# Optimization experiments

Measured on AMD Instinct MI355X. Metric: run time of the kernel, lower is better.

Reference implementation:

```python
import jax, jax.numpy as jnp
import numpy as np

H, W, C = 56, 56, 192
WS, SS = 7, 3          # window_size, shift_size
NH, HD = 6, 32         # num_heads, head_dim
N = WS * WS            # tokens per window = 49
HIDDEN = 4 * C
EPS = 1e-5


def _rel_pos_index():
    coords = np.stack(np.meshgrid(np.arange(WS), np.arange(WS), indexing='ij'))  # (2,ws,ws)
    flat = coords.reshape(2, -1)
    rel = flat[:, :, None] - flat[:, None, :]            # (2,N,N)
    rel = rel.transpose(1, 2, 0)
    rel[:, :, 0] += WS - 1
    rel[:, :, 1] += WS - 1
    rel[:, :, 0] *= 2 * WS - 1
    return rel.sum(-1)                                   # (N,N) int


def _attn_mask():
    img = np.zeros((H, W))
    cnt = 0
    for hs in (slice(0, -WS), slice(-WS, -SS), slice(-SS, None)):
        for ws_ in (slice(0, -WS), slice(-WS, -SS), slice(-SS, None)):
            img[hs, ws_] = cnt
            cnt += 1
    mw = img.reshape(H // WS, WS, W // WS, WS).transpose(0, 2, 1, 3).reshape(-1, N)  # (nW,N)
    diff = mw[:, None, :] - mw[:, :, None]
    return np.where(diff != 0, -100.0, 0.0).astype(np.float32)  # (nW,N,N)


REL_IDX = jnp.asarray(_rel_pos_index())
ATTN_MASK = jnp.asarray(_attn_mask())


def _ln(x, w, b):
    mu = x.mean(-1, keepdims=True)
    var = ((x - mu) ** 2).mean(-1, keepdims=True)
    return (x - mu) * jax.lax.rsqrt(var + EPS) * w + b


def _window_partition(x):
    # (B,H,W,C) -> (B*nW, N, C)
    B = x.shape[0]
    x = x.reshape(B, H // WS, WS, W // WS, WS, C)
    x = x.transpose(0, 1, 3, 2, 4, 5)
    return x.reshape(-1, N, C)


def _window_reverse(win, B):
    # (B*nW, N, C) -> (B,H,W,C)
    x = win.reshape(B, H // WS, W // WS, WS, WS, C)
    x = x.transpose(0, 1, 3, 2, 4, 5)
    return x.reshape(B, H, W, C)


def setup_inputs() -> dict:
    key = jax.random.key(0)
    ks = jax.random.split(key, 16)
    s = 0.02
    return {
        'x': jax.random.normal(ks[0], (64, H * W, C), jnp.float32),
        'norm1_w': jnp.ones((C,), jnp.float32),
        'norm1_b': jnp.zeros((C,), jnp.float32),
        'qkv_w': jax.random.normal(ks[1], (C, 3 * C), jnp.float32) * s,
        'qkv_b': jnp.zeros((3 * C,), jnp.float32),
        'rpb': jax.random.normal(ks[2], ((2 * WS - 1) ** 2, NH), jnp.float32) * s,
        'proj_w': jax.random.normal(ks[3], (C, C), jnp.float32) * s,
        'proj_b': jnp.zeros((C,), jnp.float32),
        'norm2_w': jnp.ones((C,), jnp.float32),
        'norm2_b': jnp.zeros((C,), jnp.float32),
        'fc1_w': jax.random.normal(ks[4], (C, HIDDEN), jnp.float32) * s,
        'fc1_b': jnp.zeros((HIDDEN,), jnp.float32),
        'fc2_w': jax.random.normal(ks[5], (HIDDEN, C), jnp.float32) * s,
        'fc2_b': jnp.zeros((C,), jnp.float32),
    }


def reference(x, norm1_w, norm1_b, qkv_w, qkv_b, rpb, proj_w, proj_b,
              norm2_w, norm2_b, fc1_w, fc1_b, fc2_w, fc2_b):
    B = x.shape[0]
    nW = (H // WS) * (W // WS)
    shortcut = x
    h = _ln(x, norm1_w, norm1_b).reshape(B, H, W, C)
    # cyclic shift
    h = jnp.roll(h, shift=(-SS, -SS), axis=(1, 2))
    xw = _window_partition(h)                                   # (B*nW, N, C)
    # windowed MHA
    qkv = (xw @ qkv_w + qkv_b).reshape(-1, N, 3, NH, HD).transpose(2, 0, 3, 1, 4)
    q, k, v = qkv[0], qkv[1], qkv[2]                            # (Bn, NH, N, HD)
    scale = HD ** -0.5
    attn = jnp.einsum('bhnd,bhmd->bhnm', q * scale, k)          # (Bn, NH, N, N)
    bias = rpb[REL_IDX.reshape(-1)].reshape(N, N, NH).transpose(2, 0, 1)
    attn = attn + bias[None]
    attn = attn.reshape(B, nW, NH, N, N) + ATTN_MASK[None, :, None]
    attn = jax.nn.softmax(attn.reshape(-1, NH, N, N), axis=-1)
    out = jnp.einsum('bhnm,bhmd->bhnd', attn, v)
    out = out.transpose(0, 2, 1, 3).reshape(-1, N, C)
    out = out @ proj_w + proj_b
    # reverse windows + un-shift
    h = _window_reverse(out, B)
    h = jnp.roll(h, shift=(SS, SS), axis=(1, 2)).reshape(B, H * W, C)
    x = shortcut + h
    # MLP (exact GELU, as torch nn.GELU default)
    m = _ln(x, norm2_w, norm2_b)
    m = jax.nn.gelu(m @ fc1_w + fc1_b, approximate=False)
    m = m @ fc2_w + fc2_b
    return x + m
```

## Files before the change

kernel.cpp:

```cpp
#include <hip/hip_runtime.h>
#include <hip/hip_bf16.h>

typedef __hip_bfloat16 bf16;
typedef __attribute__((ext_vector_type(8))) short short8;
typedef __attribute__((ext_vector_type(4))) short short4v;
typedef __attribute__((ext_vector_type(4))) float floatx4;

__device__ __forceinline__ floatx4 mfma16(short8 a, short8 b, floatx4 c) {
  return __builtin_amdgcn_mfma_f32_16x16x32_bf16(a, b, c, 0, 0, 0);
}

__device__ __forceinline__ float wave_sum(float v) {
#pragma unroll
  for (int off = 1; off < 64; off <<= 1) v += __shfl_xor(v, off);
  return v;
}

__device__ __forceinline__ void gload16(const void* g, void* l) {
  __builtin_amdgcn_global_load_lds(
      (const __attribute__((address_space(1))) unsigned int*)g,
      (__attribute__((address_space(3))) unsigned int*)l, 16, 0, 0);
}

__device__ __forceinline__ short8 lds_frag(const char* base, int row, int kb) {
  return *(const short8*)(base + row * 384 + (kb ^ ((row & 7) << 4)));
}
__device__ __forceinline__ short8 lds_frag128(const char* base, int row, int kb) {
  return *(const short8*)(base + row * 128 + (kb ^ ((row & 7) << 4)));
}

__global__ __launch_bounds__(256) void k_wt(const float* __restrict__ w,
                                            bf16* __restrict__ wt, int K, int N) {
  int id = blockIdx.x * 256 + threadIdx.x;
  if (id < K * N) {
    int n = id / K;
    int k = id - n * K;
    wt[id] = __float2bfloat16(w[(long)k * N + n]);
  }
}

template <bool GATHER>
__global__ __launch_bounds__(256) void k_ln(const float* __restrict__ xin,
                                            const float* __restrict__ w,
                                            const float* __restrict__ b,
                                            bf16* __restrict__ out) {
  const int lane = threadIdx.x & 63;
  const long row = (long)blockIdx.x * 4 + (threadIdx.x >> 6);
  long srow;
  if (GATHER) {
    int win = (int)(row / 49);
    int token = (int)(row - (long)win * 49);
    int bimg = win >> 6, wi = (win & 63) >> 3, wj = win & 7;
    int ti = token / 7, tj = token - ti * 7;
    int h = wi * 7 + ti + 3; if (h >= 56) h -= 56;
    int ww = wj * 7 + tj + 3; if (ww >= 56) ww -= 56;
    srow = (long)bimg * 3136 + h * 56 + ww;
  } else {
    srow = row;
  }
  const float* src = xin + srow * 192;
  float v0 = src[lane], v1 = src[lane + 64], v2 = src[lane + 128];
  float mu = wave_sum(v0 + v1 + v2) * (1.f / 192.f);
  float d0 = v0 - mu, d1 = v1 - mu, d2 = v2 - mu;
  float var = wave_sum(d0 * d0 + d1 * d1 + d2 * d2) * (1.f / 192.f);
  float rs = rsqrtf(var + 1e-5f);
  bf16* dst = out + row * 192;
  dst[lane]       = __float2bfloat16(d0 * rs * w[lane] + b[lane]);
  dst[lane + 64]  = __float2bfloat16(d1 * rs * w[lane + 64] + b[lane + 64]);
  dst[lane + 128] = __float2bfloat16(d2 * rs * w[lane + 128] + b[lane + 128]);
}

template <int EPI>
__global__ __launch_bounds__(256, 3) void k_gemm(const bf16* __restrict__ A,
                                                 const bf16* __restrict__ Bt,
                                                 const float* __restrict__ bias,
                                                 bf16* __restrict__ Cbf,
                                                 float* __restrict__ Cfp,
                                                 const float* __restrict__ res,
                                                 int Ncols, int K, long row0) {
  __shared__ __align__(16) char As[64 * 384];
  __shared__ __align__(16) char Bs[64 * 384];
  const int t = threadIdx.x;
  const int lane = t & 63, wid = t >> 6;
  const int lanelo = lane & 15, quad = lane >> 4;
  const long m0 = (long)blockIdx.x * 64;
  const int n0 = blockIdx.y * 64;
  const int wm = (wid >> 1) * 32, wn = (wid & 1) * 32;

  floatx4 acc[2][2];
#pragma unroll
  for (int i = 0; i < 2; i++)
#pragma unroll
    for (int j = 0; j < 2; j++) acc[i][j] = (floatx4){0.f, 0.f, 0.f, 0.f};

  const char* Ab = (const char*)(A + m0 * (long)K);
  const char* Bb = (const char*)(Bt + (long)n0 * K);
  const int ldab = 2 * K;

  for (int k0b = 0; k0b < 2 * K; k0b += 384) {
    __syncthreads();
#pragma unroll
    for (int i = 0; i < 6; i++) {
      int c = i * 256 + t;
      int r = c / 24;
      int j = c - r * 24;
      int be = (j * 16) ^ ((r & 7) << 4);
      gload16(Ab + (long)r * ldab + k0b + be, As + c * 16);
      gload16(Bb + (long)r * ldab + k0b + be, Bs + c * 16);
    }
    __syncthreads();

#pragma unroll
    for (int kk = 0; kk < 6; kk++) {
      const int kb = kk * 64 + quad * 16;
      short8 a0 = lds_frag(As, wm + lanelo, kb);
      short8 a1 = lds_frag(As, wm + 16 + lanelo, kb);
      short8 b0 = lds_frag(Bs, wn + lanelo, kb);
      short8 b1 = lds_frag(Bs, wn + 16 + lanelo, kb);
      acc[0][0] = mfma16(a0, b0, acc[0][0]);
      acc[0][1] = mfma16(a0, b1, acc[0][1]);
      acc[1][0] = mfma16(a1, b0, acc[1][0]);
      acc[1][1] = mfma16(a1, b1, acc[1][1]);
    }
  }

#pragma unroll
  for (int mi = 0; mi < 2; mi++) {
#pragma unroll
    for (int reg = 0; reg < 4; reg++) {
      const long r = m0 + wm + mi * 16 + quad * 4 + reg;
      long orow = r;
      if (EPI == 2) {
        const long rg = row0 + r;
        int win = (int)(rg / 49);
        int token = (int)(rg - (long)win * 49);
        int bimg = win >> 6, wi = (win & 63) >> 3, wj = win & 7;
        int ti = token / 7, tj = token - ti * 7;
        int h = wi * 7 + ti + 3; if (h >= 56) h -= 56;
        int ww = wj * 7 + tj + 3; if (ww >= 56) ww -= 56;
        orow = (long)bimg * 3136 + h * 56 + ww;
      }
#pragma unroll
      for (int ni = 0; ni < 2; ni++) {
        const int c = n0 + wn + ni * 16 + lanelo;
        float v = acc[mi][ni][reg] + bias[c];
        if (EPI == 0) {
          Cbf[r * Ncols + c] = __float2bfloat16(v);
        } else if (EPI == 1) {
          v = 0.5f * v * (1.f + erff(v * 0.70710678118654752f));
          Cbf[r * Ncols + c] = __float2bfloat16(v);
        } else if (EPI == 2) {
          Cfp[orow * 192 + c] = v + res[orow * 192 + c];
        } else {
          Cfp[r * 192 + c] = v + res[r * 192 + c];
        }
      }
    }
  }
}

__global__ __launch_bounds__(256, 2) void k_attn2(const bf16* __restrict__ xw,
                                                  const bf16* __restrict__ wq,
                                                  const float* __restrict__ qkvb,
                                                  const float* __restrict__ rpb,
                                                  bf16* __restrict__ attC) {
  __shared__ __align__(16) bf16 smem[4 * 7424];
  const int t = threadIdx.x, lane = t & 63, wid = t >> 6;
  const int lanelo = lane & 15, quad = lane >> 4;
  const int unit = blockIdx.x * 4 + wid;
  const int win = unit / 6, head = unit - win * 6;
  bf16* Qs = smem + wid * 7424;
  bf16* Ks = Qs + 2560;
  bf16* Vt = Qs + 5120;
  bf16* Ps = Qs;
  const long rowbase = (long)win * 49;

  const int w_in = win & 63, wiw = w_in >> 3, wjw = w_in & 7;
  int cTi[4], cTj[4], cLab[4];
  bool cval[4];
#pragma unroll
  for (int ni = 0; ni < 4; ni++) {
    int j = ni * 16 + lanelo;
    cval[ni] = (j < 49);
    if (j > 48) j = 48;
    int ti = j / 7, tj = j - ti * 7;
    int rr = wiw * 7 + ti, cc = wjw * 7 + tj;
    cTi[ni] = ti; cTj[ni] = tj;
    cLab[ni] = ((rr < 49) ? 0 : (rr < 53 ? 1 : 2)) * 3 +
               ((cc < 49) ? 0 : (cc < 53 ? 1 : 2));
  }

  const float scale = 0.17677669529663687f;

  {
    floatx4 aq[4][6];
#pragma unroll
    for (int mi = 0; mi < 4; mi++)
#pragma unroll
      for (int ni = 0; ni < 6; ni++) aq[mi][ni] = (floatx4){0.f, 0.f, 0.f, 0.f};
#pragma unroll
    for (int kk = 0; kk < 6; kk++) {
      const int kb = kk * 64 + quad * 16;
      short8 af[4];
#pragma unroll
      for (int mi = 0; mi < 4; mi++)
        af[mi] = *(const short8*)((const char*)xw +
                                  (rowbase + mi * 16 + lanelo) * 384 + kb);
#pragma unroll
      for (int ni = 0; ni < 6; ni++) {
        const int wrow = (ni >> 1) * 192 + head * 32 + (ni & 1) * 16 + lanelo;
        short8 bf = *(const short8*)((const char*)wq + (long)wrow * 384 + kb);
#pragma unroll
        for (int mi = 0; mi < 4; mi++) aq[mi][ni] = mfma16(af[mi], bf, aq[mi][ni]);
      }
    }
#pragma unroll
    for (int ni = 0; ni < 6; ni++) {
      const int p = ni >> 1;
      const int d = (ni & 1) * 16 + lanelo;
      const float bb = qkvb[p * 192 + head * 32 + d];
      if (p < 2) {
        bf16* dst = (p == 0) ? Qs : Ks;
#pragma unroll
        for (int mi = 0; mi < 4; mi++)
#pragma unroll
          for (int reg = 0; reg < 4; reg++) {
            int tok = mi * 16 + quad * 4 + reg;
            dst[tok * 40 + d] = __float2bfloat16(aq[mi][ni][reg] + bb);
          }
      } else {
#pragma unroll
        for (int mi = 0; mi < 4; mi++) {
          union { short4v s; bf16 hh[4]; } pv;
#pragma unroll
          for (int reg = 0; reg < 4; reg++)
            pv.hh[reg] = __float2bfloat16(aq[mi][ni][reg] + bb);
          *(short4v*)(&Vt[d * 72 + mi * 16 + quad * 4]) = pv.s;
        }
      }
    }
  }

  float rinv[16];
  {
    floatx4 aS[4][4];
#pragma unroll
    for (int mi = 0; mi < 4; mi++) {
      short8 aqf = *(const short8*)(&Qs[(mi * 16 + lanelo) * 40 + quad * 8]);
#pragma unroll
      for (int ni = 0; ni < 4; ni++) {
        short8 bk = *(const short8*)(&Ks[(ni * 16 + lanelo) * 40 + quad * 8]);
        aS[mi][ni] = mfma16(aqf, bk, (floatx4){0.f, 0.f, 0.f, 0.f});
      }
    }
#pragma unroll
    for (int mi = 0; mi < 4; mi++) {
#pragma unroll
      for (int reg = 0; reg < 4; reg++) {
        int i = mi * 16 + quad * 4 + reg;
        if (i > 48) i = 48;
        int ti = i / 7, tj = i - ti * 7;
        int rr = wiw * 7 + ti, cc = wjw * 7 + tj;
        int rlab = ((rr < 49) ? 0 : (rr < 53 ? 1 : 2)) * 3 +
                   ((cc < 49) ? 0 : (cc < 53 ? 1 : 2));
        float sv[4];
        float mx = -1e30f;
#pragma unroll
        for (int ni = 0; ni < 4; ni++) {
          float s;
          if (cval[ni]) {
            int ridx = (ti - cTi[ni] + 6) * 13 + (tj - cTj[ni] + 6);
            float bb = rpb[ridx * 6 + head];
            if (rlab != cLab[ni]) bb -= 100.f;
            s = aS[mi][ni][reg] * scale + bb;
          } else {
            s = -1e30f;
          }
          sv[ni] = s;
          mx = fmaxf(mx, s);
        }
        mx = fmaxf(mx, __shfl_xor(mx, 1));
        mx = fmaxf(mx, __shfl_xor(mx, 2));
        mx = fmaxf(mx, __shfl_xor(mx, 4));
        mx = fmaxf(mx, __shfl_xor(mx, 8));
        float sum = 0.f;
#pragma unroll
        for (int ni = 0; ni < 4; ni++) {
          float p = __expf(sv[ni] - mx);
          sv[ni] = p;
          sum += p;
        }
        sum += __shfl_xor(sum, 1);
        sum += __shfl_xor(sum, 2);
        sum += __shfl_xor(sum, 4);
        sum += __shfl_xor(sum, 8);
        rinv[mi * 4 + reg] = 1.f / sum;
#pragma unroll
        for (int ni = 0; ni < 4; ni++) aS[mi][ni][reg] = sv[ni];
      }
    }
#pragma unroll
    for (int mi = 0; mi < 4; mi++)
#pragma unroll
      for (int ni = 0; ni < 4; ni++)
#pragma unroll
        for (int reg = 0; reg < 4; reg++)
          Ps[(mi * 16 + quad * 4 + reg) * 72 + ni * 16 + lanelo] =
              __float2bfloat16(aS[mi][ni][reg]);
  }

  floatx4 aO[4][2];
#pragma unroll
  for (int mi = 0; mi < 4; mi++)
#pragma unroll
    for (int ni = 0; ni < 2; ni++) aO[mi][ni] = (floatx4){0.f, 0.f, 0.f, 0.f};
#pragma unroll
  for (int ks = 0; ks < 2; ks++) {
#pragma unroll
    for (int mi = 0; mi < 4; mi++) {
      short8 ap = *(const short8*)(&Ps[(mi * 16 + lanelo) * 72 + ks * 32 + quad * 8]);
#pragma unroll
      for (int ni = 0; ni < 2; ni++) {
        short8 bv = *(const short8*)(&Vt[(ni * 16 + lanelo) * 72 + ks * 32 + quad * 8]);
        aO[mi][ni] = mfma16(ap, bv, aO[mi][ni]);
      }
    }
  }

#pragma unroll
  for (int mi = 0; mi < 4; mi++)
#pragma unroll
    for (int reg = 0; reg < 4; reg++) {
      int i = mi * 16 + quad * 4 + reg;
      if (i < 49) {
        float rv = rinv[mi * 4 + reg];
#pragma unroll
        for (int ni = 0; ni < 2; ni++) {
          int d = ni * 16 + lanelo;
          attC[(rowbase + i) * 192 + head * 32 + d] =
              __float2bfloat16(aO[mi][ni][reg] * rv);
        }
      }
    }
}

__global__ __launch_bounds__(256, 4) void k_mlp(float* xres,
                                                const float* __restrict__ lw,
                                                const float* __restrict__ lb,
                                                const bf16* __restrict__ w1t,
                                                const float* __restrict__ b1,
                                                const bf16* __restrict__ w2t,
                                                const float* __restrict__ b2) {
  __shared__ __align__(16) char As[64 * 384];
  __shared__ __align__(16) char Hs[2][64 * 128];
  const int t = threadIdx.x, lane = t & 63, wid = t >> 6;
  const int lanelo = lane & 15, quad = lane >> 4;
  const long row0 = (long)blockIdx.x * 64;

  for (int i = 0; i < 16; i++) {
    int r = wid * 16 + i;
    const float* src = xres + (row0 + r) * 192;
    float v0 = src[lane], v1 = src[lane + 64], v2 = src[lane + 128];
    float mu = wave_sum(v0 + v1 + v2) * (1.f / 192.f);
    float d0 = v0 - mu, d1 = v1 - mu, d2 = v2 - mu;
    float var = wave_sum(d0 * d0 + d1 * d1 + d2 * d2) * (1.f / 192.f);
    float rs = rsqrtf(var + 1e-5f);
    int sw = (r & 7) << 4;
    *(bf16*)(As + r * 384 + ((2 * lane) ^ sw)) =
        __float2bfloat16(d0 * rs * lw[lane] + lb[lane]);
    *(bf16*)(As + r * 384 + ((128 + 2 * lane) ^ sw)) =
        __float2bfloat16(d1 * rs * lw[lane + 64] + lb[lane + 64]);
    *(bf16*)(As + r * 384 + ((256 + 2 * lane) ^ sw)) =
        __float2bfloat16(d2 * rs * lw[lane + 128] + lb[lane + 128]);
  }

  floatx4 acc2[4][3];
#pragma unroll
  for (int mi = 0; mi < 4; mi++)
#pragma unroll
    for (int ni = 0; ni < 3; ni++) acc2[mi][ni] = (floatx4){0.f, 0.f, 0.f, 0.f};

  __syncthreads();

  const int hcol = wid * 16 + lanelo;
  const int ocol0 = wid * 48;

  for (int nc = 0; nc < 12; nc++) {
    const char* w1p = (const char*)w1t + (long)(nc * 64 + hcol) * 384;
    floatx4 acc1[4];
#pragma unroll
    for (int mi = 0; mi < 4; mi++) acc1[mi] = (floatx4){0.f, 0.f, 0.f, 0.f};
#pragma unroll
    for (int kk = 0; kk < 6; kk++) {
      const int kb = kk * 64 + quad * 16;
      short8 bf = *(const short8*)(w1p + kb);
#pragma unroll
      for (int mi = 0; mi < 4; mi++) {
        short8 af = lds_frag(As, mi * 16 + lanelo, kb);
        acc1[mi] = mfma16(af, bf, acc1[mi]);
      }
    }

    char* H = Hs[nc & 1];
    const float b1v = b1[nc * 64 + hcol];
#pragma unroll
    for (int mi = 0; mi < 4; mi++)
#pragma unroll
      for (int reg = 0; reg < 4; reg++) {
        int r = mi * 16 + quad * 4 + reg;
        float v = acc1[mi][reg] + b1v;
        v = 0.5f * v * (1.f + erff(v * 0.70710678118654752f));
        *(bf16*)(H + r * 128 + ((2 * hcol) ^ ((r & 7) << 4))) =
            __float2bfloat16(v);
      }
    __syncthreads();

#pragma unroll
    for (int ks = 0; ks < 2; ks++) {
      const int kb = ks * 64 + quad * 16;
      short8 ha[4];
#pragma unroll
      for (int mi = 0; mi < 4; mi++)
        ha[mi] = lds_frag128(H, mi * 16 + lanelo, kb);
#pragma unroll
      for (int ni = 0; ni < 3; ni++) {
        short8 bv = *(const short8*)((const char*)w2t +
                                     (long)(ocol0 + ni * 16 + lanelo) * 1536 +
                                     nc * 128 + kb);
#pragma unroll
        for (int mi = 0; mi < 4; mi++)
          acc2[mi][ni] = mfma16(ha[mi], bv, acc2[mi][ni]);
      }
    }
  }

#pragma unroll
  for (int mi = 0; mi < 4; mi++)
#pragma unroll
    for (int ni = 0; ni < 3; ni++) {
      const int c = ocol0 + ni * 16 + lanelo;
      const float b2v = b2[c];
#pragma unroll
      for (int reg = 0; reg < 4; reg++) {
        const long g = (row0 + mi * 16 + quad * 4 + reg) * 192 + c;
        xres[g] = acc2[mi][ni][reg] + b2v + xres[g];
      }
    }
}

extern "C" void kernel_launch(void* const* d_in, const int* in_sizes, int n_in,
                              void* d_out, int out_size, void* d_ws, size_t ws_size,
                              hipStream_t stream) {
  const float* x     = (const float*)d_in[0];
  const float* n1w   = (const float*)d_in[1];
  const float* n1b   = (const float*)d_in[2];
  const float* qkvw  = (const float*)d_in[3];
  const float* qkvb  = (const float*)d_in[4];
  const float* rpb   = (const float*)d_in[5];
  const float* projw = (const float*)d_in[6];
  const float* projb = (const float*)d_in[7];
  const float* n2w   = (const float*)d_in[8];
  const float* n2b   = (const float*)d_in[9];
  const float* fc1w  = (const float*)d_in[10];
  const float* fc1b  = (const float*)d_in[11];
  const float* fc2w  = (const float*)d_in[12];
  const float* fc2b  = (const float*)d_in[13];
  float* outf = (float*)d_out;

  char* ws = (char*)d_ws;
  bf16* xw      = (bf16*)(ws + 0);
  bf16* attC    = (bf16*)(ws + 77070336LL);
  bf16* wt_qkv  = (bf16*)(ws + 154140672LL);
  bf16* wt_proj = (bf16*)(ws + 154140672LL + 221184LL);
  bf16* wt_fc1  = (bf16*)(ws + 154140672LL + 294912LL);
  bf16* wt_fc2  = (bf16*)(ws + 154140672LL + 589824LL);

  k_wt<<<dim3((192 * 576 + 255) / 256), 256, 0, stream>>>(qkvw, wt_qkv, 192, 576);
  k_wt<<<dim3((192 * 192 + 255) / 256), 256, 0, stream>>>(projw, wt_proj, 192, 192);
  k_wt<<<dim3((192 * 768 + 255) / 256), 256, 0, stream>>>(fc1w, wt_fc1, 192, 768);
  k_wt<<<dim3((768 * 192 + 255) / 256), 256, 0, stream>>>(fc2w, wt_fc2, 768, 192);

  k_ln<true><<<dim3(50176), 256, 0, stream>>>(x, n1w, n1b, xw);

  k_attn2<<<dim3(6144), 256, 0, stream>>>(xw, wt_qkv, qkvb, rpb, attC);

  k_gemm<2><<<dim3(3136, 3), 256, 0, stream>>>(attC, wt_proj, projb, nullptr,
                                               outf, x, 192, 192, 0);

  k_mlp<<<dim3(3136), 256, 0, stream>>>(outf, n2w, n2b, wt_fc1, fc1b,
                                        wt_fc2, fc2b);
}
```

Before: 993.1 us.

## Precompute bias+mask tables per window class and split QKV projection into QK and V passes

A new small kernel builds a 64x64 table of relative-position bias plus shift mask (with -inf padding) for each of the 4 window classes and 6 heads. The attention kernel then reads one table entry instead of doing per-element index arithmetic and gathering from rpb. It also splits the fused QKV accumulation into separate QK and V passes, which lowers live accumulator registers but reloads the xw fragments twice. The table is stored in the output buffer as scratch before the output is written.

```diff
diff --git a/kernel.cpp b/kernel.cpp
--- a/kernel.cpp
+++ b/kernel.cpp
@@ -36,6 +36,30 @@
     int n = id / K;
     int k = id - n * K;
     wt[id] = __float2bfloat16(w[(long)k * N + n]);
+  }
+}
+
+__global__ __launch_bounds__(256) void k_bias(const float* __restrict__ rpb,
+                                              float* __restrict__ Btab) {
+  const int bh = blockIdx.x;
+  const int cls = bh / 6, head = bh - cls * 6;
+  const bool rb = (cls & 2) != 0, cb = (cls & 1) != 0;
+  for (int idx = threadIdx.x; idx < 4096; idx += 256) {
+    int i = idx >> 6, j = idx & 63;
+    float v;
+    if (j >= 49) {
+      v = -1e30f;
+    } else {
+      int ie = (i > 48) ? 48 : i;
+      int ti = ie / 7, tj = ie - ti * 7;
+      int cti = j / 7, ctj = j - cti * 7;
+      int ridx = (ti - cti + 6) * 13 + (tj - ctj + 6);
+      v = rpb[ridx * 6 + head];
+      int rlab = (rb ? (ti < 4 ? 1 : 2) : 0) * 3 + (cb ? (tj < 4 ? 1 : 2) : 0);
+      int clab = (rb ? (cti < 4 ? 1 : 2) : 0) * 3 + (cb ? (ctj < 4 ? 1 : 2) : 0);
+      if (rlab != clab) v -= 100.f;
+    }
+    Btab[(long)bh * 4096 + i * 64 + j] = v;
   }
 }
 
@@ -162,7 +186,7 @@
 __global__ __launch_bounds__(256, 2) void k_attn2(const bf16* __restrict__ xw,
                                                   const bf16* __restrict__ wq,
                                                   const float* __restrict__ qkvb,
-                                                  const float* __restrict__ rpb,
+                                                  const float* __restrict__ Btab,
                                                   bf16* __restrict__ attC) {
   __shared__ __align__(16) bf16 smem[4 * 7424];
   const int t = threadIdx.x, lane = t & 63, wid = t >> 6;
@@ -175,29 +199,18 @@
   bf16* Ps = Qs;
   const long rowbase = (long)win * 49;
 
-  const int w_in = win & 63, wiw = w_in >> 3, wjw = w_in & 7;
-  int cTi[4], cTj[4], cLab[4];
-  bool cval[4];
-#pragma unroll
-  for (int ni = 0; ni < 4; ni++) {
-    int j = ni * 16 + lanelo;
-    cval[ni] = (j < 49);
-    if (j > 48) j = 48;
-    int ti = j / 7, tj = j - ti * 7;
-    int rr = wiw * 7 + ti, cc = wjw * 7 + tj;
-    cTi[ni] = ti; cTj[ni] = tj;
-    cLab[ni] = ((rr < 49) ? 0 : (rr < 53 ? 1 : 2)) * 3 +
-               ((cc < 49) ? 0 : (cc < 53 ? 1 : 2));
-  }
+  const int w_in = win & 63;
+  const int cls = (((w_in >> 3) == 7) ? 2 : 0) + (((w_in & 7) == 7) ? 1 : 0);
+  const float* Bt = Btab + (long)(cls * 6 + head) * 4096;
 
   const float scale = 0.17677669529663687f;
 
   {
-    floatx4 aq[4][6];
+    floatx4 aq[4][4];
 #pragma unroll
     for (int mi = 0; mi < 4; mi++)
 #pragma unroll
-      for (int ni = 0; ni < 6; ni++) aq[mi][ni] = (floatx4){0.f, 0.f, 0.f, 0.f};
+      for (int ni = 0; ni < 4; ni++) aq[mi][ni] = (floatx4){0.f, 0.f, 0.f, 0.f};
 #pragma unroll
     for (int kk = 0; kk < 6; kk++) {
       const int kb = kk * 64 + quad * 16;
@@ -207,7 +220,7 @@
         af[mi] = *(const short8*)((const char*)xw +
                                   (rowbase + mi * 16 + lanelo) * 384 + kb);
 #pragma unroll
-      for (int ni = 0; ni < 6; ni++) {
+      for (int ni = 0; ni < 4; ni++) {
         const int wrow = (ni >> 1) * 192 + head * 32 + (ni & 1) * 16 + lanelo;
         short8 bf = *(const short8*)((const char*)wq + (long)wrow * 384 + kb);
 #pragma unroll
@@ -215,28 +228,54 @@
       }
     }
 #pragma unroll
-    for (int ni = 0; ni < 6; ni++) {
+    for (int ni = 0; ni < 4; ni++) {
       const int p = ni >> 1;
       const int d = (ni & 1) * 16 + lanelo;
       const float bb = qkvb[p * 192 + head * 32 + d];
-      if (p < 2) {
-        bf16* dst = (p == 0) ? Qs : Ks;
-#pragma unroll
-        for (int mi = 0; mi < 4; mi++)
-#pragma unroll
-          for (int reg = 0; reg < 4; reg++) {
-            int tok = mi * 16 + quad * 4 + reg;
-            dst[tok * 40 + d] = __float2bfloat16(aq[mi][ni][reg] + bb);
-          }
-      } else {
-#pragma unroll
-        for (int mi = 0; mi < 4; mi++) {
-          union { short4v s; bf16 hh[4]; } pv;
-#pragma unroll
-          for (int reg = 0; reg < 4; reg++)
-            pv.hh[reg] = __float2bfloat16(aq[mi][ni][reg] + bb);
-          *(short4v*)(&Vt[d * 72 + mi * 16 + quad * 4]) = pv.s;
+      bf16* dst = (p == 0) ? Qs : Ks;
+#pragma unroll
+      for (int mi = 0; mi < 4; mi++)
+#pragma unroll
+        for (int reg = 0; reg < 4; reg++) {
+          int tok = mi * 16 + quad * 4 + reg;
+          dst[tok * 40 + d] = __float2bfloat16(aq[mi][ni][reg] + bb);
         }
+    }
+  }
+
+  {
+    floatx4 av[4][2];
+#pragma unroll
+    for (int mi = 0; mi < 4; mi++)
+#pragma unroll
+      for (int ni = 0; ni < 2; ni++) av[mi][ni] = (floatx4){0.f, 0.f, 0.f, 0.f};
+#pragma unroll
+    for (int kk = 0; kk < 6; kk++) {
+      const int kb = kk * 64 + quad * 16;
+      short8 af[4];
+#pragma unroll
+      for (int mi = 0; mi < 4; mi++)
+        af[mi] = *(const short8*)((const char*)xw +
+                                  (rowbase + mi * 16 + lanelo) * 384 + kb);
+#pragma unroll
+      for (int ni = 0; ni < 2; ni++) {
+        const int wrow = 384 + head * 32 + ni * 16 + lanelo;
+        short8 bf = *(const short8*)((const char*)wq + (long)wrow * 384 + kb);
+#pragma unroll
+        for (int mi = 0; mi < 4; mi++) av[mi][ni] = mfma16(af[mi], bf, av[mi][ni]);
+      }
+    }
+#pragma unroll
+    for (int ni = 0; ni < 2; ni++) {
+      const int d = ni * 16 + lanelo;
+      const float bb = qkvb[384 + head * 32 + d];
+#pragma unroll
+      for (int mi = 0; mi < 4; mi++) {
+        union { short4v s; bf16 hh[4]; } pv;
+#pragma unroll
+        for (int reg = 0; reg < 4; reg++)
+          pv.hh[reg] = __float2bfloat16(av[mi][ni][reg] + bb);
+        *(short4v*)(&Vt[d * 72 + mi * 16 + quad * 4]) = pv.s;
       }
     }
   }
@@ -257,25 +296,13 @@
     for (int mi = 0; mi < 4; mi++) {
 #pragma unroll
       for (int reg = 0; reg < 4; reg++) {
-        int i = mi * 16 + quad * 4 + reg;
-        if (i > 48) i = 48;
-        int ti = i / 7, tj = i - ti * 7;
-        int rr = wiw * 7 + ti, cc = wjw * 7 + tj;
-        int rlab = ((rr < 49) ? 0 : (rr < 53 ? 1 : 2)) * 3 +
-                   ((cc < 49) ? 0 : (cc < 53 ? 1 : 2));
+        const int i = mi * 16 + quad * 4 + reg;
+        const float* bp = Bt + i * 64;
         float sv[4];
         float mx = -1e30f;
 #pragma unroll
         for (int ni = 0; ni < 4; ni++) {
-          float s;
-          if (cval[ni]) {
-            int ridx = (ti - cTi[ni] + 6) * 13 + (tj - cTj[ni] + 6);
-            float bb = rpb[ridx * 6 + head];
-            if (rlab != cLab[ni]) bb -= 100.f;
-            s = aS[mi][ni][reg] * scale + bb;
-          } else {
-            s = -1e30f;
-          }
+          float s = aS[mi][ni][reg] * scale + bp[ni * 16 + lanelo];
           sv[ni] = s;
           mx = fmaxf(mx, s);
         }
@@ -474,15 +501,18 @@
   bf16* wt_proj = (bf16*)(ws + 154140672LL + 221184LL);
   bf16* wt_fc1  = (bf16*)(ws + 154140672LL + 294912LL);
   bf16* wt_fc2  = (bf16*)(ws + 154140672LL + 589824LL);
+  float* Btab   = (float*)d_out;
 
   k_wt<<<dim3((192 * 576 + 255) / 256), 256, 0, stream>>>(qkvw, wt_qkv, 192, 576);
   k_wt<<<dim3((192 * 192 + 255) / 256), 256, 0, stream>>>(projw, wt_proj, 192, 192);
   k_wt<<<dim3((192 * 768 + 255) / 256), 256, 0, stream>>>(fc1w, wt_fc1, 192, 768);
   k_wt<<<dim3((768 * 192 + 255) / 256), 256, 0, stream>>>(fc2w, wt_fc2, 768, 192);
 
+  k_bias<<<dim3(24), 256, 0, stream>>>(rpb, Btab);
+
   k_ln<true><<<dim3(50176), 256, 0, stream>>>(x, n1w, n1b, xw);
 
-  k_attn2<<<dim3(6144), 256, 0, stream>>>(xw, wt_qkv, qkvb, rpb, attC);
+  k_attn2<<<dim3(6144), 256, 0, stream>>>(xw, wt_qkv, qkvb, Btab, attC);
 
   k_gemm<2><<<dim3(3136, 3), 256, 0, stream>>>(attC, wt_proj, projb, nullptr,
                                                outf, x, 192, 192, 0);
```

Measured after the change: 988.4 us. Within noise of the previous version (-0.5%).
